# Optimization experiments

Measured on AMD Instinct MI355X. Metric: run time of the kernel, lower is better.

The kernel has to match this reference:

```python
import jax, jax.numpy as jnp
import numpy as np

B, C, H, W = 8, 64, 64, 64
OUT = 256
N_PAIRS = C * (C + 1) // 2          # 2080 upper-triangular (incl diag) products
N_IN = C + N_PAIRS                  # 2144 conv input channels


def setup_inputs() -> dict:
    key = jax.random.key(0)
    k1, k2 = jax.random.split(key)
    x = jax.random.normal(k1, (B, C, H, W), dtype=jnp.float32)
    fc_w = jax.random.normal(k2, (OUT, N_IN), dtype=jnp.float32) * 0.02
    return {"x": x, "fc_w": fc_w}


def reference(x, fc_w):
    # Upper-triangular indices (row-major, incl diagonal) == get_square_indices(C)
    ii, jj = np.triu_indices(x.shape[1])
    # Per-pixel outer product restricted to the needed triangular terms.
    quad = x[:, ii] * x[:, jj]                  # [B, C(C+1)/2, H, W]
    y = jnp.concatenate([x, quad], axis=1)      # [B, C(C+3)/2, H, W]
    # 1x1 conv, bias=False -> pointwise channel GEMM
    return jnp.einsum('bchw,oc->bohw', y, fc_w)
```

## Files before the change

kernel.cpp:

```cpp
#include <hip/hip_runtime.h>
#include <hip/hip_bf16.h>

using u16 = unsigned short;
using u32 = unsigned int;

typedef __attribute__((ext_vector_type(8))) short s16x8;
typedef __attribute__((ext_vector_type(4))) float f32x4;
typedef __attribute__((ext_vector_type(4))) u32   u32x4;

#define NQ   74
#define NRUN 296
#define BM   128

__device__ __forceinline__ u16 f2bf_rne(float f) {
    u32 u = __builtin_bit_cast(u32, f);
    u32 r = u + 0x7fffu + ((u >> 16) & 1u);
    return (u16)(r >> 16);
}
__device__ __forceinline__ float bf2f(u16 u) {
    u32 v = ((u32)u) << 16;
    return __builtin_bit_cast(float, v);
}

__device__ __forceinline__ void run_decode(int r, int& i, int& j0) {
    if (r < 8) { i = 64; j0 = r << 3; return; }
    int rr = r - 8;
    int ii = 0;
    while (true) { int cnt = 8 - (ii >> 3); if (rr < cnt) break; rr -= cnt; ++ii; }
    i = ii;
    j0 = ((ii >> 3) << 3) + (rr << 3);
}

__global__ __launch_bounds__(256) void pack_w(const float* __restrict__ fcw,
                                              s16x8* __restrict__ wpk) {
    int tid = blockIdx.x * 256 + threadIdx.x;
    if (tid >= NQ * 1024) return;
    int l = tid & 63;
    int t = (tid >> 6) & 15;
    int q = tid >> 10;
    int g = l >> 4;
    int n = t * 16 + (l & 15);
    int i, j0; run_decode(q * 4 + g, i, j0);
    const float* row = fcw + n * 2144;
    short w8[8];
    #pragma unroll
    for (int e = 0; e < 8; ++e) {
        int j = j0 + e;
        float w;
        if (i == 64)    w = row[j];
        else if (j < i) w = 0.f;
        else            w = row[64 + i * 64 - ((i * (i - 1)) >> 1) + (j - i)];
        w8[e] = (short)f2bf_rne(w);
    }
    s16x8 v = { w8[0], w8[1], w8[2], w8[3], w8[4], w8[5], w8[6], w8[7] };
    wpk[tid] = v;
}

#define LOADW(Q, WF) do {                                                    \
    const s16x8* bp_ = wpk + ((((Q) * 16) + wn4) << 6) + l;                  \
    WF[0] = bp_[0]; WF[1] = bp_[64]; WF[2] = bp_[128]; WF[3] = bp_[192];     \
} while (0)

#define GEN(Q, BUF) do {                                                     \
    u16 ij_ = runtab[(Q) * 4 + g2];                                          \
    int i_ = ij_ >> 8, j0_ = ij_ & 255;                                      \
    float fi_ = bf2f(x_lds[xmb + ((i_ & 63) ^ sw)]);                         \
    if (i_ >= 64) fi_ = 1.0f;                                                \
    s16x8 vj_ = *(const s16x8*)(x_lds + xmb + (j0_ ^ sw));                   \
    u32 pk_[4];                                                              \
    _Pragma("unroll")                                                        \
    for (int d_ = 0; d_ < 4; ++d_) {                                         \
        float p0_ = fi_ * bf2f((u16)vj_[2 * d_]);                            \
        float p1_ = fi_ * bf2f((u16)vj_[2 * d_ + 1]);                        \
        pk_[d_] = __builtin_amdgcn_perm(__builtin_bit_cast(u32, p1_),        \
                                        __builtin_bit_cast(u32, p0_),        \
                                        0x07060302u);                        \
    }                                                                        \
    u32x4 pv_ = { pk_[0], pk_[1], pk_[2], pk_[3] };                          \
    ybuf[BUF][ygidx] = __builtin_bit_cast(s16x8, pv_);                       \
} while (0)

#define CONSUME(BUF, WF) do {                                                \
    s16x8 yf_[4];                                                            \
    _Pragma("unroll")                                                        \
    for (int mi_ = 0; mi_ < 4; ++mi_) yf_[mi_] = ybuf[BUF][ycbase + mi_ * 16]; \
    _Pragma("unroll")                                                        \
    for (int mi_ = 0; mi_ < 4; ++mi_)                                        \
        _Pragma("unroll")                                                    \
        for (int ni_ = 0; ni_ < 4; ++ni_)                                    \
            acc[mi_][ni_] = __builtin_amdgcn_mfma_f32_16x16x32_bf16(         \
                WF[ni_], yf_[mi_], acc[mi_][ni_], 0, 0, 0);                  \
} while (0)

__global__ __launch_bounds__(512, 2)
void quad_gemm(const float* __restrict__ x, const s16x8* __restrict__ wpk,
               float* __restrict__ out) {
    __shared__ __align__(16) u16 x_lds[BM * 64];
    __shared__ u16 runtab[NRUN];
    __shared__ s16x8 ybuf[2][512];

    const int t   = threadIdx.x;
    const int l   = t & 63;
    const int wv  = t >> 6;
    const int wm  = wv >> 2;
    const int wn4 = (wv & 3) << 2;
    const int lan = l & 15, gk = l >> 4;
    const int ycbase = (gk << 7) + wm * 64 + lan;
    const int g2 = t & 3, m2 = t >> 2;
    const int xmb = m2 << 6, sw = (m2 & 7) << 3;
    const int ygidx = (g2 << 7) + m2;

    const int pix0 = blockIdx.x * BM;
    const int b   = pix0 >> 12;
    const int hw0 = pix0 & 4095;
    const float* xb = x + ((size_t)b << 18) + hw0;

    if (t < NRUN) {
        int i, j0; run_decode(t, i, j0);
        runtab[t] = (u16)((i << 8) | j0);
    }

    {
        int c = t >> 3, s = t & 7;
        const float* xc = xb + c * 4096 + s * 16;
        #pragma unroll
        for (int p4 = 0; p4 < 4; ++p4) {
            f32x4 v = *(const f32x4*)(xc + p4 * 4);
            #pragma unroll
            for (int e = 0; e < 4; ++e) {
                int m = s * 16 + p4 * 4 + e;
                x_lds[(m << 6) + (c ^ ((m & 7) << 3))] = f2bf_rne(v[e]);
            }
        }
    }

    f32x4 acc[4][4];
    #pragma unroll
    for (int mi = 0; mi < 4; ++mi)
        #pragma unroll
        for (int ni = 0; ni < 4; ++ni)
            acc[mi][ni] = (f32x4){0.f, 0.f, 0.f, 0.f};

    s16x8 W0[4], W1[4];

    __syncthreads();
    GEN(0, 0);
    LOADW(0, W0);
    __syncthreads();

    for (int q = 0; q < NQ; q += 2) {
        LOADW(q + 1, W1);
        GEN(q + 1, 1);
        CONSUME(0, W0);
        __syncthreads();
        if (q + 2 < NQ) { LOADW(q + 2, W0); GEN(q + 2, 0); }
        CONSUME(1, W1);
        __syncthreads();
    }

    float* ob = out + ((size_t)b << 20) + hw0;
    #pragma unroll
    for (int mi = 0; mi < 4; ++mi) {
        int m = wm * 64 + mi * 16 + lan;
        #pragma unroll
        for (int ni = 0; ni < 4; ++ni) {
            int o = (wn4 + ni) * 16 + gk * 4;
            #pragma unroll
            for (int p = 0; p < 4; ++p)
                ob[(size_t)(o + p) * 4096 + m] = acc[mi][ni][p];
        }
    }
}

extern "C" void kernel_launch(void* const* d_in, const int* in_sizes, int n_in,
                              void* d_out, int out_size, void* d_ws, size_t ws_size,
                              hipStream_t stream) {
    const float* x   = (const float*)d_in[0];
    const float* fcw = (const float*)d_in[1];
    float* out = (float*)d_out;
    s16x8* wpk = (s16x8*)d_ws;

    hipLaunchKernelGGL(pack_w, dim3(NQ * 4), dim3(256), 0, stream, fcw, wpk);
    hipLaunchKernelGGL(quad_gemm, dim3(256), dim3(512), 0, stream,
                       x, (const s16x8*)wpk, out);
}
```

Before: 119.3 us.

## Split output channels across blocks and generate quad operands in registers

The GEMM is restructured so that each block computes 128 pixels by 128 output channels with 256 threads, and the grid doubles to 512 blocks. Each wave now generates its own bf16 quadratic products straight into MFMA operand registers, which removes the shared ybuf staging buffer and the per-step __syncthreads. Weight fragments are double-buffered in registers. The costs are that each x tile is loaded and converted twice (once per channel half), each wave holds more accumulators, and pack_w is relaunched with one 1024-thread block per q.

```diff
diff --git a/kernel.cpp b/kernel.cpp
--- a/kernel.cpp
+++ b/kernel.cpp
@@ -10,7 +10,6 @@
 
 #define NQ   74
 #define NRUN 296
-#define BM   128
 
 __device__ __forceinline__ u16 f2bf_rne(float f) {
     u32 u = __builtin_bit_cast(u32, f);
@@ -31,16 +30,21 @@
     j0 = ((ii >> 3) << 3) + (rr << 3);
 }
 
-__global__ __launch_bounds__(256) void pack_w(const float* __restrict__ fcw,
-                                              s16x8* __restrict__ wpk) {
-    int tid = blockIdx.x * 256 + threadIdx.x;
-    if (tid >= NQ * 1024) return;
-    int l = tid & 63;
-    int t = (tid >> 6) & 15;
-    int q = tid >> 10;
-    int g = l >> 4;
-    int n = t * 16 + (l & 15);
-    int i, j0; run_decode(q * 4 + g, i, j0);
+__global__ __launch_bounds__(1024)
+void pack_w(const float* __restrict__ fcw, s16x8* __restrict__ wpk) {
+    __shared__ u16 runs4[4];
+    const int q = blockIdx.x;
+    const int t = threadIdx.x;
+    if (t < 4) {
+        int i, j0; run_decode(q * 4 + t, i, j0);
+        runs4[t] = (u16)((i << 8) | j0);
+    }
+    __syncthreads();
+    const int l = t & 63;
+    const int g = l >> 4;
+    const int n = ((t >> 6) << 4) + (l & 15);
+    const u16 ij = runs4[g];
+    const int i = ij >> 8, j0 = ij & 255;
     const float* row = fcw + n * 2144;
     short w8[8];
     #pragma unroll
@@ -53,118 +57,113 @@
         w8[e] = (short)f2bf_rne(w);
     }
     s16x8 v = { w8[0], w8[1], w8[2], w8[3], w8[4], w8[5], w8[6], w8[7] };
-    wpk[tid] = v;
+    wpk[q * 1024 + t] = v;
 }
 
-#define LOADW(Q, WF) do {                                                    \
-    const s16x8* bp_ = wpk + ((((Q) * 16) + wn4) << 6) + l;                  \
-    WF[0] = bp_[0]; WF[1] = bp_[64]; WF[2] = bp_[128]; WF[3] = bp_[192];     \
+#define STAGE(IJ, Y, W, Q) do {                                              \
+    const int i_ = (IJ) >> 8, j0_ = (IJ) & 255;                              \
+    _Pragma("unroll")                                                        \
+    for (int mi_ = 0; mi_ < 2; ++mi_) {                                      \
+        u16 fb_ = x_lds[mb[mi_] + ((i_ & 63) ^ sw)];                         \
+        s16x8 vj_ = *(const s16x8*)(x_lds + mb[mi_] + (j0_ ^ sw));           \
+        float fi_ = (i_ >= 64) ? 1.0f : bf2f(fb_);                           \
+        u32 pk_[4];                                                          \
+        _Pragma("unroll")                                                    \
+        for (int d_ = 0; d_ < 4; ++d_) {                                     \
+            float p0_ = fi_ * bf2f((u16)vj_[2 * d_]);                        \
+            float p1_ = fi_ * bf2f((u16)vj_[2 * d_ + 1]);                    \
+            pk_[d_] = __builtin_amdgcn_perm(__builtin_bit_cast(u32, p1_),    \
+                                            __builtin_bit_cast(u32, p0_),    \
+                                            0x07060302u);                    \
+        }                                                                    \
+        u32x4 pv_ = { pk_[0], pk_[1], pk_[2], pk_[3] };                      \
+        Y[mi_] = __builtin_bit_cast(s16x8, pv_);                             \
+    }                                                                        \
+    _Pragma("unroll")                                                        \
+    for (int ni_ = 0; ni_ < 8; ++ni_) W[ni_] = wb[(Q) * 1024 + ni_ * 64];    \
 } while (0)
 
-#define GEN(Q, BUF) do {                                                     \
-    u16 ij_ = runtab[(Q) * 4 + g2];                                          \
-    int i_ = ij_ >> 8, j0_ = ij_ & 255;                                      \
-    float fi_ = bf2f(x_lds[xmb + ((i_ & 63) ^ sw)]);                         \
-    if (i_ >= 64) fi_ = 1.0f;                                                \
-    s16x8 vj_ = *(const s16x8*)(x_lds + xmb + (j0_ ^ sw));                   \
-    u32 pk_[4];                                                              \
+#define MFMAQ(Y, W) do {                                                     \
     _Pragma("unroll")                                                        \
-    for (int d_ = 0; d_ < 4; ++d_) {                                         \
-        float p0_ = fi_ * bf2f((u16)vj_[2 * d_]);                            \
-        float p1_ = fi_ * bf2f((u16)vj_[2 * d_ + 1]);                        \
-        pk_[d_] = __builtin_amdgcn_perm(__builtin_bit_cast(u32, p1_),        \
-                                        __builtin_bit_cast(u32, p0_),        \
-                                        0x07060302u);                        \
-    }                                                                        \
-    u32x4 pv_ = { pk_[0], pk_[1], pk_[2], pk_[3] };                          \
-    ybuf[BUF][ygidx] = __builtin_bit_cast(s16x8, pv_);                       \
+    for (int mi_ = 0; mi_ < 2; ++mi_)                                        \
+        _Pragma("unroll")                                                    \
+        for (int ni_ = 0; ni_ < 8; ++ni_)                                    \
+            acc[mi_][ni_] = __builtin_amdgcn_mfma_f32_16x16x32_bf16(         \
+                W[ni_], Y[mi_], acc[mi_][ni_], 0, 0, 0);                     \
 } while (0)
 
-#define CONSUME(BUF, WF) do {                                                \
-    s16x8 yf_[4];                                                            \
-    _Pragma("unroll")                                                        \
-    for (int mi_ = 0; mi_ < 4; ++mi_) yf_[mi_] = ybuf[BUF][ycbase + mi_ * 16]; \
-    _Pragma("unroll")                                                        \
-    for (int mi_ = 0; mi_ < 4; ++mi_)                                        \
-        _Pragma("unroll")                                                    \
-        for (int ni_ = 0; ni_ < 4; ++ni_)                                    \
-            acc[mi_][ni_] = __builtin_amdgcn_mfma_f32_16x16x32_bf16(         \
-                WF[ni_], yf_[mi_], acc[mi_][ni_], 0, 0, 0);                  \
-} while (0)
-
-__global__ __launch_bounds__(512, 2)
+__global__ __launch_bounds__(256, 2)
 void quad_gemm(const float* __restrict__ x, const s16x8* __restrict__ wpk,
                float* __restrict__ out) {
-    __shared__ __align__(16) u16 x_lds[BM * 64];
+    __shared__ __align__(16) u16 x_lds[128 * 64];
     __shared__ u16 runtab[NRUN];
-    __shared__ s16x8 ybuf[2][512];
 
     const int t   = threadIdx.x;
     const int l   = t & 63;
     const int wv  = t >> 6;
-    const int wm  = wv >> 2;
-    const int wn4 = (wv & 3) << 2;
     const int lan = l & 15, gk = l >> 4;
-    const int ycbase = (gk << 7) + wm * 64 + lan;
-    const int g2 = t & 3, m2 = t >> 2;
-    const int xmb = m2 << 6, sw = (m2 & 7) << 3;
-    const int ygidx = (g2 << 7) + m2;
 
-    const int pix0 = blockIdx.x * BM;
-    const int b   = pix0 >> 12;
-    const int hw0 = pix0 & 4095;
-    const float* xb = x + ((size_t)b << 18) + hw0;
+    const int mtile = blockIdx.x >> 1;
+    const int nb    = blockIdx.x & 1;
+    const int pix0  = mtile * 128;
+    const int b     = pix0 >> 12;
+    const int hw0   = pix0 & 4095;
 
-    if (t < NRUN) {
-        int i, j0; run_decode(t, i, j0);
-        runtab[t] = (u16)((i << 8) | j0);
+    for (int r = t; r < NRUN; r += 256) {
+        int i, j0; run_decode(r, i, j0);
+        runtab[r] = (u16)((i << 8) | j0);
     }
 
     {
-        int c = t >> 3, s = t & 7;
-        const float* xc = xb + c * 4096 + s * 16;
+        const int c = t >> 2, s = t & 3;
+        const float* xc = x + ((size_t)b << 18) + (size_t)c * 4096 + hw0 + s * 32;
         #pragma unroll
-        for (int p4 = 0; p4 < 4; ++p4) {
+        for (int p4 = 0; p4 < 8; ++p4) {
             f32x4 v = *(const f32x4*)(xc + p4 * 4);
             #pragma unroll
             for (int e = 0; e < 4; ++e) {
-                int m = s * 16 + p4 * 4 + e;
+                int m = s * 32 + p4 * 4 + e;
                 x_lds[(m << 6) + (c ^ ((m & 7) << 3))] = f2bf_rne(v[e]);
             }
         }
     }
 
-    f32x4 acc[4][4];
+    f32x4 acc[2][8];
     #pragma unroll
-    for (int mi = 0; mi < 4; ++mi)
+    for (int mi = 0; mi < 2; ++mi)
         #pragma unroll
-        for (int ni = 0; ni < 4; ++ni)
+        for (int ni = 0; ni < 8; ++ni)
             acc[mi][ni] = (f32x4){0.f, 0.f, 0.f, 0.f};
 
-    s16x8 W0[4], W1[4];
+    const int mb[2] = { (wv * 32 + lan) << 6, (wv * 32 + 16 + lan) << 6 };
+    const int sw    = (lan & 7) << 3;
+    const s16x8* wb = wpk + nb * 512 + l;
 
     __syncthreads();
-    GEN(0, 0);
-    LOADW(0, W0);
-    __syncthreads();
 
-    for (int q = 0; q < NQ; q += 2) {
-        LOADW(q + 1, W1);
-        GEN(q + 1, 1);
-        CONSUME(0, W0);
-        __syncthreads();
-        if (q + 2 < NQ) { LOADW(q + 2, W0); GEN(q + 2, 0); }
-        CONSUME(1, W1);
-        __syncthreads();
+    s16x8 Ya[2], Wa[8], Yb[2], Wb[8];
+    int ija = runtab[0 * 4 + gk];
+    int ijb = runtab[1 * 4 + gk];
+    STAGE(ija, Ya, Wa, 0);
+    for (int q = 0; q + 2 < NQ; q += 2) {
+        ija = runtab[(q + 2) * 4 + gk];
+        STAGE(ijb, Yb, Wb, q + 1);
+        MFMAQ(Ya, Wa);
+        ijb = runtab[(q + 3) * 4 + gk];
+        STAGE(ija, Ya, Wa, q + 2);
+        MFMAQ(Yb, Wb);
     }
+    STAGE(ijb, Yb, Wb, NQ - 1);
+    MFMAQ(Ya, Wa);
+    MFMAQ(Yb, Wb);
 
     float* ob = out + ((size_t)b << 20) + hw0;
     #pragma unroll
-    for (int mi = 0; mi < 4; ++mi) {
-        int m = wm * 64 + mi * 16 + lan;
+    for (int mi = 0; mi < 2; ++mi) {
+        const int m = wv * 32 + mi * 16 + lan;
         #pragma unroll
-        for (int ni = 0; ni < 4; ++ni) {
-            int o = (wn4 + ni) * 16 + gk * 4;
+        for (int ni = 0; ni < 8; ++ni) {
+            const int o = nb * 128 + ni * 16 + gk * 4;
             #pragma unroll
             for (int p = 0; p < 4; ++p)
                 ob[(size_t)(o + p) * 4096 + m] = acc[mi][ni][p];
@@ -180,7 +179,7 @@
     float* out = (float*)d_out;
     s16x8* wpk = (s16x8*)d_ws;
 
-    hipLaunchKernelGGL(pack_w, dim3(NQ * 4), dim3(256), 0, stream, fcw, wpk);
-    hipLaunchKernelGGL(quad_gemm, dim3(256), dim3(512), 0, stream,
+    hipLaunchKernelGGL(pack_w, dim3(NQ), dim3(1024), 0, stream, fcw, wpk);
+    hipLaunchKernelGGL(quad_gemm, dim3(512), dim3(256), 0, stream,
                        x, (const s16x8*)wpk, out);
 }
```

After: 116.5 us. 2.4% less time.
